# Kernel tuning notes

Measured on AMD Instinct MI355X. Metric: run time of the kernel, lower is better.

## Reference

```python
import jax, jax.numpy as jnp
import numpy as np
import math

H = 16
D_MODEL = 1024
D_K = D_MODEL // H


def setup_inputs() -> dict:
    key0 = jax.random.key(0)
    ks = jax.random.split(key0, 20)
    B, S, D = 4, 1024, D_MODEL
    inp = {
        'query': jax.random.normal(ks[0], (B, S, D), jnp.float32),
        'key': jax.random.normal(ks[1], (B, S, D), jnp.float32),
        'value': jax.random.normal(ks[2], (B, S, D), jnp.float32),
        'mask': jnp.ones((B, 1, S), jnp.int32),
    }
    sc = 1.0 / math.sqrt(D)
    # linears[0]=key proj, [1]=value proj, [2]=query proj, [3]=output proj (per source)
    names = ['W_k', 'W_v', 'W_q', 'W_o', 'W_fq', 'W_fg']
    for i, n in enumerate(names):
        inp[n] = jax.random.normal(ks[3 + i], (D, D), jnp.float32) * sc
        inp['b' + n[1:]] = jnp.zeros((D,), jnp.float32)
    inp['up'] = jax.random.normal(ks[10], (H, 1, D_K), jnp.float32) * sc
    inp['uz'] = jax.random.normal(ks[11], (H, 1, D_K), jnp.float32) * sc
    return inp


def _heads(x, B, S):
    return jnp.transpose(x.reshape(B, S, H, D_K), (0, 2, 1, 3))  # [B,h,S,d_k]


def reference(query, key, value, mask, W_k, b_k, W_v, b_v, W_q, b_q, W_o, b_o, W_fq, b_fq, W_fg, b_fg, up, uz):
    B, S, D = query.shape
    k = _heads(key @ W_k.T + b_k, B, S)
    v = _heads(value @ W_v.T + b_v, B, S)
    q_lin = query @ W_q.T + b_q  # [B,S,D]
    # Gaussian focus bias
    glo = jnp.mean(q_lin, axis=1, keepdims=True)  # [B,1,D]
    c = jnp.tanh(q_lin @ W_fq.T + b_fq + (glo @ W_fg.T + b_fg))
    c = _heads(c, B, S)  # [B,h,S,d_k]
    p = jnp.sum(c * up, axis=-1)  # [B,h,S]
    z = jnp.sum(c * uz, axis=-1)
    P = jax.nn.sigmoid(p) * S
    Z = jax.nn.sigmoid(z) * S
    j = jnp.arange(S, dtype=P.dtype)  # key positions
    G = -((j[None, None, None, :] - P[..., None]) ** 2) * 2.0 / (Z[..., None] ** 2)  # [B,h,S,S]
    q = _heads(q_lin, B, S)
    scores = jnp.einsum('bhqd,bhkd->bhqk', q, k) / math.sqrt(D_K) + G
    scores = jnp.where(mask[:, None] == 0, jnp.float32(-1e15), scores)
    attn = jax.nn.softmax(scores, axis=-1)
    x = jnp.einsum('bhqk,bhkd->bhqd', attn, v)
    x = jnp.transpose(x, (0, 2, 1, 3)).reshape(B, S, D)
    out = x @ W_o.T + b_o
    return out, jnp.mean(attn, axis=1)
```

## Files before the change

kernel.cpp:

```cpp
#include <hip/hip_runtime.h>
#include <hip/hip_bf16.h>
#include <math.h>

typedef __attribute__((ext_vector_type(8))) short short8;
typedef __attribute__((ext_vector_type(4))) short short4v;
typedef __attribute__((ext_vector_type(4))) float f32x4;
typedef unsigned short u16;

#define SC2 0.18033688011112042f
#define L2E 1.4426950408889634f

__device__ __forceinline__ u16 f2bf(float f) {
  union { float f; unsigned u; } v; v.f = f;
  unsigned u = v.u + 0x7fffu + ((v.u >> 16) & 1u);
  return (u16)(u >> 16);
}
__device__ __forceinline__ float bf2f(u16 h) {
  union { unsigned u; float f; } v; v.u = ((unsigned)h) << 16;
  return v.f;
}
__device__ __forceinline__ float fexp2(float x) {
  float r; asm("v_exp_f32 %0, %1" : "=v"(r) : "v"(x)); return r;
}
__device__ __forceinline__ void gl_lds16(const u16* g, u16* l) {
  __builtin_amdgcn_global_load_lds(
      (const __attribute__((address_space(1))) void*)g,
      (__attribute__((address_space(3))) void*)l, 16, 0, 0);
}

__device__ __forceinline__ size_t KFoff(int b, int h, int j, int d) {
  return ((((size_t)(b * 16 + h) * 64 + (j >> 4)) * 2 + (d >> 5)) * 64
          + ((d >> 3) & 3) * 16 + (j & 15)) * 8 + (d & 7);
}
__device__ __forceinline__ size_t VFoff(int b, int h, int j, int d) {
  return ((((size_t)(b * 16 + h) * 4 + (d >> 4)) * 32 + (j >> 5)) * 64
          + ((j >> 3) & 3) * 16 + (d & 15)) * 8 + (j & 7);
}

__global__ __launch_bounds__(256) void cvt_all(
    const float* __restrict__ q, const float* __restrict__ k, const float* __restrict__ v,
    const float* __restrict__ w0, const float* __restrict__ w1, const float* __restrict__ w2,
    const float* __restrict__ w3, const float* __restrict__ w4,
    u16* __restrict__ qb, u16* __restrict__ kb, u16* __restrict__ vb,
    u16* __restrict__ w0b, u16* __restrict__ w1b, u16* __restrict__ w2b,
    u16* __restrict__ w3b, u16* __restrict__ w4b) {
  int bid = blockIdx.x;
  const float* s; u16* d; int base;
  if (bid < 2048)      { s = q; d = qb; base = bid; }
  else if (bid < 4096) { s = k; d = kb; base = bid - 2048; }
  else if (bid < 6144) { s = v; d = vb; base = bid - 4096; }
  else {
    int t2 = bid - 6144; int wi = t2 >> 9; base = t2 & 511;
    if (wi == 0)      { s = w0; d = w0b; }
    else if (wi == 1) { s = w1; d = w1b; }
    else if (wi == 2) { s = w2; d = w2b; }
    else if (wi == 3) { s = w3; d = w3b; }
    else              { s = w4; d = w4b; }
  }
  size_t idx = (size_t)base * 2048 + (size_t)threadIdx.x * 8;
  float4 a = *(const float4*)(s + idx);
  float4 b = *(const float4*)(s + idx + 4);
  short8 o;
  o[0] = (short)f2bf(a.x); o[1] = (short)f2bf(a.y); o[2] = (short)f2bf(a.z); o[3] = (short)f2bf(a.w);
  o[4] = (short)f2bf(b.x); o[5] = (short)f2bf(b.y); o[6] = (short)f2bf(b.z); o[7] = (short)f2bf(b.w);
  *(short8*)(d + idx) = o;
}

#define GEMM_CORE(A_, Bw_)                                                              \
  f32x4 acc[4][4];                                                                      \
  _Pragma("unroll") for (int m = 0; m < 4; ++m)                                         \
    _Pragma("unroll") for (int n = 0; n < 4; ++n)                                       \
      acc[m][n] = (f32x4){0.f, 0.f, 0.f, 0.f};                                          \
  for (int k0 = 0; k0 < 1024; k0 += 64) {                                               \
    _Pragma("unroll") for (int p = 0; p < 4; ++p) {                                     \
      int idx = p * 256 + tid;                                                          \
      int row = idx >> 3, slot = idx & 7;                                               \
      gl_lds16(A_ + (size_t)(m0 + row) * 1024 + k0 + ((slot ^ (row & 7)) * 8), As + idx * 8); \
    }                                                                                   \
    _Pragma("unroll") for (int p = 0; p < 4; ++p) {                                     \
      int idx = p * 256 + tid;                                                          \
      int row = idx >> 3, slot = idx & 7;                                               \
      gl_lds16(Bw_ + (size_t)(n0 + row) * 1024 + k0 + ((slot ^ (row & 7)) * 8), Bs + idx * 8); \
    }                                                                                   \
    __syncthreads();                                                                    \
    _Pragma("unroll") for (int kk = 0; kk < 2; ++kk) {                                  \
      short8 af[4], bf[4];                                                              \
      _Pragma("unroll") for (int m = 0; m < 4; ++m) {                                   \
        int row = wrow + m * 16 + c;                                                    \
        af[m] = *(const short8*)(As + row * 64 + (((kk * 4 + g) ^ (row & 7)) * 8));     \
      }                                                                                 \
      _Pragma("unroll") for (int n = 0; n < 4; ++n) {                                   \
        int row = wcol + n * 16 + c;                                                    \
        bf[n] = *(const short8*)(Bs + row * 64 + (((kk * 4 + g) ^ (row & 7)) * 8));     \
      }                                                                                 \
      _Pragma("unroll") for (int m = 0; m < 4; ++m)                                     \
        _Pragma("unroll") for (int n = 0; n < 4; ++n)                                   \
          acc[m][n] = __builtin_amdgcn_mfma_f32_16x16x32_bf16(af[m], bf[n], acc[m][n], 0, 0, 0); \
    }                                                                                   \
    __syncthreads();                                                                    \
  }

__global__ __launch_bounds__(256, 2)
void proj_qkv(const u16* __restrict__ qb, const u16* __restrict__ kb, const u16* __restrict__ vb,
              const u16* __restrict__ wqb, const u16* __restrict__ wkb, const u16* __restrict__ wvb,
              const float* __restrict__ bq, const float* __restrict__ bk, const float* __restrict__ bv,
              u16* __restrict__ Ql, u16* __restrict__ Kf, u16* __restrict__ Vf) {
  __shared__ u16 As[128 * 64];
  __shared__ u16 Bs[128 * 64];
  const int z = blockIdx.z;
  const u16* A  = (z == 0) ? kb : (z == 1) ? vb : qb;
  const u16* Bw = (z == 0) ? wkb : (z == 1) ? wvb : wqb;
  const float* bias = (z == 0) ? bk : (z == 1) ? bv : bq;
  const int tid = threadIdx.x;
  const int l = tid & 63, w = tid >> 6;
  const int m0 = blockIdx.x * 128, n0 = blockIdx.y * 128;
  const int wrow = (w & 1) * 64, wcol = (w >> 1) * 64;
  const int g = l >> 4, c = l & 15;

  GEMM_CORE(A, Bw)

#pragma unroll
  for (int n = 0; n < 4; ++n) {
    int col = n0 + wcol + n * 16 + c;
    float bv_ = bias[col];
    int hh = col >> 6, dd = col & 63;
#pragma unroll
    for (int m = 0; m < 4; ++m) {
#pragma unroll
      for (int r = 0; r < 4; ++r) {
        int rowg = m0 + wrow + m * 16 + g * 4 + r;
        float val = acc[m][n][r] + bv_;
        int bb = rowg >> 10, jj = rowg & 1023;
        if (z == 0)      Kf[KFoff(bb, hh, jj, dd)] = f2bf(val);
        else if (z == 1) Vf[VFoff(bb, hh, jj, dd)] = f2bf(val);
        else             Ql[(size_t)rowg * 1024 + col] = f2bf(val);
      }
    }
  }
}

__global__ __launch_bounds__(256, 2)
void gemm_tanh(const u16* __restrict__ A, const u16* __restrict__ Bw,
               const float* __restrict__ gb, u16* __restrict__ Cout) {
  __shared__ u16 As[128 * 64];
  __shared__ u16 Bs[128 * 64];
  const int tid = threadIdx.x;
  const int l = tid & 63, w = tid >> 6;
  const int m0 = blockIdx.x * 128, n0 = blockIdx.y * 128;
  const int wrow = (w & 1) * 64, wcol = (w >> 1) * 64;
  const int g = l >> 4, c = l & 15;

  GEMM_CORE(A, Bw)

#pragma unroll
  for (int n = 0; n < 4; ++n) {
    int col = n0 + wcol + n * 16 + c;
    float bv = gb[(m0 >> 10) * 1024 + col];
#pragma unroll
    for (int m = 0; m < 4; ++m) {
#pragma unroll
      for (int r = 0; r < 4; ++r) {
        int rowg = m0 + wrow + m * 16 + g * 4 + r;
        Cout[(size_t)rowg * 1024 + col] = f2bf(tanhf(acc[m][n][r] + bv));
      }
    }
  }
}

__global__ __launch_bounds__(128) void glo_part_k(const u16* __restrict__ qlin, float* __restrict__ gpart) {
  int b = blockIdx.x & 3, seg = blockIdx.x >> 2;
  int t = threadIdx.x;
  float acc[8] = {0, 0, 0, 0, 0, 0, 0, 0};
  for (int s = seg * 16; s < seg * 16 + 16; ++s) {
    short8 v = *(const short8*)(qlin + (size_t)(b * 1024 + s) * 1024 + t * 8);
#pragma unroll
    for (int j = 0; j < 8; ++j) acc[j] += bf2f((u16)v[j]);
  }
#pragma unroll
  for (int j = 0; j < 8; ++j) gpart[(size_t)(seg * 4 + b) * 1024 + t * 8 + j] = acc[j];
}

__global__ __launch_bounds__(128) void glo_reduce(const float* __restrict__ gpart, float* __restrict__ glo) {
  int b = blockIdx.x & 3, cc = blockIdx.x >> 2;
  int col = cc * 128 + threadIdx.x;
  float a[8] = {0, 0, 0, 0, 0, 0, 0, 0};
#pragma unroll
  for (int s8 = 0; s8 < 8; ++s8) {
#pragma unroll
    for (int s = 0; s < 8; ++s)
      a[s] += gpart[(size_t)((s8 * 8 + s) * 4 + b) * 1024 + col];
  }
  float t = ((a[0] + a[1]) + (a[2] + a[3])) + ((a[4] + a[5]) + (a[6] + a[7]));
  glo[b * 1024 + col] = t * (1.0f / 1024.0f);
}

__global__ __launch_bounds__(256) void gbias_k(const float* __restrict__ glo, const float* __restrict__ Wfg,
                                               const float* __restrict__ bfq, const float* __restrict__ bfg,
                                               float* __restrict__ gbias) {
  __shared__ float glo_l[4096];
  int tid = threadIdx.x;
  for (int idx = tid; idx < 4096; idx += 256) glo_l[idx] = glo[idx];
  __syncthreads();
  int w = tid >> 6, l = tid & 63;
#pragma unroll
  for (int i = 0; i < 4; ++i) {
    int n = blockIdx.x * 16 + w * 4 + i;
    float a0 = 0, a1 = 0, a2 = 0, a3 = 0;
#pragma unroll
    for (int kk = 0; kk < 4; ++kk) {
      int k = kk * 256 + l * 4;
      float4 wv = *(const float4*)(Wfg + (size_t)n * 1024 + k);
      float4 g0 = *(const float4*)(&glo_l[k]);
      float4 g1 = *(const float4*)(&glo_l[1024 + k]);
      float4 g2 = *(const float4*)(&glo_l[2048 + k]);
      float4 g3 = *(const float4*)(&glo_l[3072 + k]);
      a0 += wv.x * g0.x + wv.y * g0.y + wv.z * g0.z + wv.w * g0.w;
      a1 += wv.x * g1.x + wv.y * g1.y + wv.z * g1.z + wv.w * g1.w;
      a2 += wv.x * g2.x + wv.y * g2.y + wv.z * g2.z + wv.w * g2.w;
      a3 += wv.x * g3.x + wv.y * g3.y + wv.z * g3.z + wv.w * g3.w;
    }
#pragma unroll
    for (int d = 1; d < 64; d <<= 1) {
      a0 += __shfl_xor(a0, d); a1 += __shfl_xor(a1, d);
      a2 += __shfl_xor(a2, d); a3 += __shfl_xor(a3, d);
    }
    if (l == 0) {
      float bb = bfq[n] + bfg[n];
      gbias[n] = a0 + bb; gbias[1024 + n] = a1 + bb;
      gbias[2048 + n] = a2 + bb; gbias[3072 + n] = a3 + bb;
    }
  }
}

__global__ __launch_bounds__(256) void pz_kernel(const u16* __restrict__ cbuf,
                                                 const float* __restrict__ up, const float* __restrict__ uz,
                                                 float* __restrict__ Pout, float* __restrict__ IZout) {
  __shared__ float lup[1024], luz[1024];
  int tid = threadIdx.x;
  for (int i = tid; i < 1024; i += 256) { lup[i] = up[i]; luz[i] = uz[i]; }
  __syncthreads();
  int w = tid >> 6, l = tid & 63;
  int sg = blockIdx.x * 4 + w;
  int b = sg >> 10, s = sg & 1023;
  const u16* crow = cbuf + (size_t)sg * 1024;
  for (int h = 0; h < 16; ++h) {
    float cv = bf2f(crow[h * 64 + l]);
    float pp = cv * lup[h * 64 + l];
    float zz = cv * luz[h * 64 + l];
#pragma unroll
    for (int d = 1; d < 64; d <<= 1) { pp += __shfl_xor(pp, d); zz += __shfl_xor(zz, d); }
    if (l == 0) {
      float Pv = 1024.f / (1.f + __expf(-pp));
      float Zv = 1024.f / (1.f + __expf(-zz));
      size_t o = (size_t)(b * 16 + h) * 1024 + s;
      Pout[o] = Pv;
      IZout[o] = 2.0f / (Zv * Zv) * L2E;
    }
  }
}

template<int WP>
__global__ __launch_bounds__(512, 4)
void attn_flash(const u16* __restrict__ Qlin, const u16* __restrict__ Kf, const u16* __restrict__ Vf,
                const float* __restrict__ Pbuf, const float* __restrict__ IZbuf,
                const int* __restrict__ mask,
                u16* __restrict__ xbuf, float* __restrict__ Mbuf, float* __restrict__ iLbuf,
                u16* __restrict__ Pall, float* __restrict__ mch) {
  __shared__ u16 sm16[24576];
  __shared__ float maskb_s[1024];

  const int tid = threadIdx.x;
  const int l = tid & 63, w = tid >> 6;
  const int g = l >> 4, c = l & 15;
  const int bid = blockIdx.x;
  const int bh = (bid & 7) + ((bid >> 6) << 3);
  const int qc = (bid >> 3) & 7;
  const int b = bh >> 4, h = bh & 15;
  const int q0w = qc * 128 + w * 16;

  char* ps_ = (char*)(sm16 + 16384) + w * 2048;

  const u16* KfH = Kf + (size_t)bh * 65536;
  const u16* VfH = Vf + (size_t)bh * 65536;
  const int sdt = tid >> 7, sinner = tid & 127;

#pragma unroll
  for (int i = 0; i < 2; ++i) {
    int idx = i * 512 + tid;
    maskb_s[idx] = (mask[b * 1024 + idx] == 0) ? -1.4e15f : 0.0f;
  }

  const u16* qrow = Qlin + (size_t)(b * 1024 + q0w + c) * 1024 + h * 64 + g * 8;
  short8 af0 = *(const short8*)qrow;
  short8 af1 = *(const short8*)(qrow + 32);
  float Pq[4], IZq[4];
#pragma unroll
  for (int r = 0; r < 4; ++r) {
    size_t o = (size_t)bh * 1024 + q0w + g * 4 + r;
    Pq[r] = Pbuf[o]; IZq[r] = IZbuf[o];
  }

  float m[4], lsum[4];
  f32x4 xacc[4];
#pragma unroll
  for (int r = 0; r < 4; ++r) { m[r] = -3.0e38f; lsum[r] = 0.f; }
#pragma unroll
  for (int dt = 0; dt < 4; ++dt) xacc[dt] = (f32x4){0.f, 0.f, 0.f, 0.f};

  gl_lds16(KfH + (size_t)0 * 4096 + tid * 8, sm16 + tid * 8);
  gl_lds16(VfH + ((size_t)(sdt * 32 + 0) * 512) + sinner * 8, sm16 + 4096 + tid * 8);
  __syncthreads();

  for (int jc = 0; jc < 16; ++jc) {
    const int bi = jc & 1;
    u16* Ksb = sm16 + bi * 8192;
    u16* Vsb = Ksb + 4096;
    if (jc < 15) {
      u16* Ksn = sm16 + (bi ^ 1) * 8192;
      gl_lds16(KfH + (size_t)(jc + 1) * 4096 + tid * 8, Ksn + tid * 8);
      gl_lds16(VfH + ((size_t)(sdt * 32 + (jc + 1) * 2) * 512) + sinner * 8, Ksn + 4096 + tid * 8);
    }

    f32x4 sc[4];
    float cm[4] = {-3.0e38f, -3.0e38f, -3.0e38f, -3.0e38f};
#pragma unroll
    for (int t = 0; t < 4; ++t) {
      short8 b0 = *(const short8*)(Ksb + (t * 2 + 0) * 512 + l * 8);
      short8 b1 = *(const short8*)(Ksb + (t * 2 + 1) * 512 + l * 8);
      f32x4 z = (f32x4){0.f, 0.f, 0.f, 0.f};
      z = __builtin_amdgcn_mfma_f32_16x16x32_bf16(af0, b0, z, 0, 0, 0);
      z = __builtin_amdgcn_mfma_f32_16x16x32_bf16(af1, b1, z, 0, 0, 0);
      int j = jc * 64 + t * 16 + c;
      float jf = (float)j, mbv = maskb_s[j];
#pragma unroll
      for (int r = 0; r < 4; ++r) {
        float diff = jf - Pq[r];
        float s = z[r] * SC2 + mbv - diff * diff * IZq[r];
        sc[t][r] = s;
        cm[r] = fmaxf(cm[r], s);
      }
    }
#pragma unroll
    for (int d = 1; d < 16; d <<= 1)
#pragma unroll
      for (int r = 0; r < 4; ++r) cm[r] = fmaxf(cm[r], __shfl_xor(cm[r], d));
    bool grow = (cm[0] > m[0]) | (cm[1] > m[1]) | (cm[2] > m[2]) | (cm[3] > m[3]);
    const bool resc = __any(grow);
    float scale[4], ps[4];
    if (resc) {
#pragma unroll
      for (int r = 0; r < 4; ++r) {
        float nm = fmaxf(m[r], cm[r]);
        scale[r] = fexp2(m[r] - nm);
        m[r] = nm;
      }
    }
#pragma unroll
    for (int r = 0; r < 4; ++r) ps[r] = 0.f;
#pragma unroll
    for (int t = 0; t < 4; ++t) {
#pragma unroll
      for (int r = 0; r < 4; ++r) {
        float p = fexp2(sc[t][r] - m[r]);
        ps[r] += p;
        int row = g * 4 + r;
        int byte = (row * 128 + (t * 16 + c) * 2) ^ ((row & 7) << 4);
        *(u16*)(ps_ + byte) = f2bf(p);
      }
    }
    if (resc) {
#pragma unroll
      for (int r = 0; r < 4; ++r) {
        lsum[r] = lsum[r] * scale[r] + ps[r];
#pragma unroll
        for (int dt = 0; dt < 4; ++dt) xacc[dt][r] *= scale[r];
      }
    } else {
#pragma unroll
      for (int r = 0; r < 4; ++r) lsum[r] += ps[r];
    }
    if (WP && c == 0) {
#pragma unroll
      for (int r = 0; r < 4; ++r)
        mch[((size_t)bh * 16 + jc) * 1024 + q0w + g * 4 + r] = m[r];
    }
    if (WP) {
#pragma unroll
      for (int k2 = 0; k2 < 2; ++k2) {
        int i = k2 * 512 + l * 8;
        int row = i >> 6, col = i & 63;
        int byte = (row * 128 + col * 2) ^ ((row & 7) << 4);
        short8 v = *(const short8*)(ps_ + byte);
        *(short8*)(Pall + (((size_t)bh * 16 + jc) * 1024 + q0w + row) * 64 + col) = v;
      }
    }
    short8 pa[2];
#pragma unroll
    for (int ks = 0; ks < 2; ++ks) {
      int abyte = (c * 128 + (ks * 32 + g * 8) * 2) ^ ((c & 7) << 4);
      pa[ks] = *(const short8*)(ps_ + abyte);
    }
#pragma unroll
    for (int dt = 0; dt < 4; ++dt) {
#pragma unroll
      for (int ks = 0; ks < 2; ++ks) {
        short8 vb = *(const short8*)(Vsb + (dt * 2 + ks) * 512 + l * 8);
        xacc[dt] = __builtin_amdgcn_mfma_f32_16x16x32_bf16(pa[ks], vb, xacc[dt], 0, 0, 0);
      }
    }
    __syncthreads();
  }

#pragma unroll
  for (int d = 1; d < 16; d <<= 1)
#pragma unroll
    for (int r = 0; r < 4; ++r) lsum[r] += __shfl_xor(lsum[r], d);
  float iLr[4];
#pragma unroll
  for (int r = 0; r < 4; ++r) iLr[r] = 1.0f / lsum[r];
  if (c == 0) {
#pragma unroll
    for (int r = 0; r < 4; ++r) {
      size_t o = (size_t)bh * 1024 + q0w + g * 4 + r;
      Mbuf[o] = m[r];
      iLbuf[o] = iLr[r];
    }
  }
  float* xs = (float*)sm16 + w * 1024;
#pragma unroll
  for (int dt = 0; dt < 4; ++dt)
#pragma unroll
    for (int r = 0; r < 4; ++r)
      xs[(g * 4 + r) * 64 + dt * 16 + c] = xacc[dt][r] * iLr[r];
#pragma unroll
  for (int k2 = 0; k2 < 4; ++k2) {
    int i = k2 * 256 + l * 4;
    int row = i >> 6, d0 = i & 63;
    f32x4 xv = *(const f32x4*)(xs + i);
    short4v o;
    o[0] = (short)f2bf(xv.x); o[1] = (short)f2bf(xv.y);
    o[2] = (short)f2bf(xv.z); o[3] = (short)f2bf(xv.w);
    *(short4v*)(xbuf + (size_t)(b * 1024 + q0w + row) * 1024 + h * 64 + d0) = o;
  }
}

__global__ __launch_bounds__(256, 2)
void epilogue_k(const u16* __restrict__ A, const u16* __restrict__ Bw,
                const float* __restrict__ bias, float* __restrict__ out0,
                const u16* __restrict__ Pall, const float* __restrict__ iLbuf,
                const float* __restrict__ Mbuf, const float* __restrict__ mchb,
                float* __restrict__ out2, int usePall) {
  __shared__ u16 As[128 * 64];
  __shared__ u16 Bs[128 * 64];
  const int bid = blockIdx.x;
  const int tid = threadIdx.x;
  if (bid >= 256) {
    if (!usePall) return;
    int bq = (bid - 256) * 2 + (tid >> 7);
    int b = bq >> 10, q = bq & 1023;
    int j = (tid & 127) * 8;
    int jc = j >> 6, jin = j & 63;
    float acc[8] = {0, 0, 0, 0, 0, 0, 0, 0};
    for (int h = 0; h < 16; ++h) {
      int bh = b * 16 + h;
      float M = Mbuf[(size_t)bh * 1024 + q];
      float iLh = iLbuf[(size_t)bh * 1024 + q];
      float mc = mchb[((size_t)bh * 16 + jc) * 1024 + q];
      float f = fexp2(mc - M) * iLh;
      short8 p = *(const short8*)(Pall + (((size_t)bh * 16 + jc) * 1024 + q) * 64 + jin);
#pragma unroll
      for (int i = 0; i < 8; ++i) acc[i] = fmaf(bf2f((u16)p[i]), f, acc[i]);
    }
    float* dst = out2 + (size_t)bq * 1024 + j;
#pragma unroll
    for (int i = 0; i < 8; ++i) dst[i] = acc[i] * 0.0625f;
    return;
  }
  const int l = tid & 63, w = tid >> 6;
  const int m0 = (bid & 31) * 128, n0 = (bid >> 5) * 128;
  const int wrow = (w & 1) * 64, wcol = (w >> 1) * 64;
  const int g = l >> 4, c = l & 15;

  GEMM_CORE(A, Bw)

#pragma unroll
  for (int n = 0; n < 4; ++n) {
    int col = n0 + wcol + n * 16 + c;
    float bv = bias[col];
#pragma unroll
    for (int m = 0; m < 4; ++m) {
#pragma unroll
      for (int r = 0; r < 4; ++r) {
        int rowg = m0 + wrow + m * 16 + g * 4 + r;
        out0[(size_t)rowg * 1024 + col] = acc[m][n][r] + bv;
      }
    }
  }
}

__global__ __launch_bounds__(512, 4)
void attn_mean(const u16* __restrict__ Qlin, const u16* __restrict__ Kf,
               const float* __restrict__ Pbuf, const float* __restrict__ IZbuf,
               const float* __restrict__ Mbuf, const float* __restrict__ iLbuf,
               const int* __restrict__ mask,
               float* __restrict__ out2) {
  const int tid = threadIdx.x;
  const int l = tid & 63, w = tid >> 6;
  const int g = l >> 4, c = l & 15;
  int chunk = (blockIdx.x % 8) * 64 + blockIdx.x / 8;
  const int b = chunk >> 7;
  const int qt = (chunk & 127) >> 1;
  const int jh = chunk & 1;
  const int q0 = qt * 16;
  const int jbase = jh * 512 + w * 64;

  float mb[4];
#pragma unroll
  for (int t = 0; t < 4; ++t)
    mb[t] = (mask[b * 1024 + jbase + t * 16 + c] == 0) ? -1.4e15f : 0.0f;

  f32x4 macc[4];
#pragma unroll
  for (int t = 0; t < 4; ++t) macc[t] = (f32x4){0.f, 0.f, 0.f, 0.f};

  for (int h = 0; h < 16; ++h) {
    const u16* qrow = Qlin + (size_t)(b * 1024 + q0 + c) * 1024 + h * 64 + g * 8;
    short8 af0 = *(const short8*)qrow;
    short8 af1 = *(const short8*)(qrow + 32);
    const u16* kb2 = Kf + ((size_t)((b * 16 + h) * 64 + jh * 32 + w * 4) * 2) * 512 + l * 8;
    float Pq[4], IZq[4], Mq[4], iLq[4];
#pragma unroll
    for (int r = 0; r < 4; ++r) {
      size_t o = (size_t)(b * 16 + h) * 1024 + q0 + g * 4 + r;
      Pq[r] = Pbuf[o]; IZq[r] = IZbuf[o]; Mq[r] = Mbuf[o]; iLq[r] = iLbuf[o] * 0.0625f;
    }
#pragma unroll
    for (int t = 0; t < 4; ++t) {
      short8 bf0 = *(const short8*)(kb2 + t * 1024);
      short8 bf1 = *(const short8*)(kb2 + t * 1024 + 512);
      f32x4 z = (f32x4){0.f, 0.f, 0.f, 0.f};
      z = __builtin_amdgcn_mfma_f32_16x16x32_bf16(af0, bf0, z, 0, 0, 0);
      z = __builtin_amdgcn_mfma_f32_16x16x32_bf16(af1, bf1, z, 0, 0, 0);
      float jf = (float)(jbase + t * 16 + c);
#pragma unroll
      for (int r = 0; r < 4; ++r) {
        float diff = jf - Pq[r];
        float s = z[r] * SC2 + mb[t] - diff * diff * IZq[r];
        macc[t][r] += fexp2(s - Mq[r]) * iLq[r];
      }
    }
  }
#pragma unroll
  for (int t = 0; t < 4; ++t) {
#pragma unroll
    for (int r = 0; r < 4; ++r)
      out2[(size_t)(b * 1024 + q0 + g * 4 + r) * 1024 + jbase + t * 16 + c] = macc[t][r];
  }
}

extern "C" void kernel_launch(void* const* d_in, const int* in_sizes, int n_in,
                              void* d_out, int out_size, void* d_ws, size_t ws_size,
                              hipStream_t stream) {
  const float* q   = (const float*)d_in[0];
  const float* k   = (const float*)d_in[1];
  const float* v   = (const float*)d_in[2];
  const int*   msk = (const int*)d_in[3];
  const float* Wk  = (const float*)d_in[4];  const float* bk  = (const float*)d_in[5];
  const float* Wv  = (const float*)d_in[6];  const float* bv  = (const float*)d_in[7];
  const float* Wq  = (const float*)d_in[8];  const float* bq  = (const float*)d_in[9];
  const float* Wo  = (const float*)d_in[10]; const float* bo  = (const float*)d_in[11];
  const float* Wfq = (const float*)d_in[12]; const float* bfq = (const float*)d_in[13];
  const float* Wfg = (const float*)d_in[14]; const float* bfg = (const float*)d_in[15];
  const float* up  = (const float*)d_in[16]; const float* uz  = (const float*)d_in[17];

  const size_t MB = 1u << 20;
  char* base = (char*)d_ws;
  char* p = base;
  auto take = [&](size_t n) { char* r = p; p += (n + 255) & ~(size_t)255; return r; };
  u16* Kf   = (u16*)take(8 * MB);
  u16* Ql   = (u16*)take(8 * MB);
  u16* Vf   = (u16*)take(8 * MB);
  u16* xb   = (u16*)take(8 * MB);
  u16* wob  = (u16*)take(2 * MB);
  float* Pb    = (float*)take((size_t)65536 * 4);
  float* IZb   = (float*)take((size_t)65536 * 4);
  float* Mb    = (float*)take((size_t)65536 * 4);
  float* iLb   = (float*)take((size_t)65536 * 4);
  float* mch   = (float*)take((size_t)64 * 16 * 1024 * 4);
  float* gpart = (float*)take((size_t)64 * 4 * 1024 * 4);
  float* glo   = (float*)take(4096 * 4);
  float* gbias = (float*)take(4096 * 4);
  size_t pool_off = (size_t)(p - base);
  u16* qb   = (u16*)take(8 * MB);
  u16* kb   = (u16*)take(8 * MB);
  u16* vb   = (u16*)take(8 * MB);
  u16* wkb  = (u16*)take(2 * MB);
  u16* wvb  = (u16*)take(2 * MB);
  u16* wqb  = (u16*)take(2 * MB);
  u16* wfqb = (u16*)take(2 * MB);
  u16* Cc   = (u16*)take(8 * MB);
  u16* Pall = (u16*)(base + pool_off);
  int usePall = (ws_size >= pool_off + (size_t)128 * MB) ? 1 : 0;

  float* out0 = (float*)d_out;
  float* out2 = out0 + (size_t)4 * 1024 * 1024;

  cvt_all<<<8704, 256, 0, stream>>>(q, k, v, Wk, Wv, Wq, Wfq, Wo,
                                    qb, kb, vb, wkb, wvb, wqb, wfqb, wob);
  dim3 gg3(32, 8, 3);
  proj_qkv<<<gg3, 256, 0, stream>>>(qb, kb, vb, wqb, wkb, wvb, bq, bk, bv, Ql, Kf, Vf);
  dim3 gg(32, 8);
  glo_part_k<<<256, 128, 0, stream>>>(Ql, gpart);
  glo_reduce<<<32, 128, 0, stream>>>(gpart, glo);
  gbias_k<<<64, 256, 0, stream>>>(glo, Wfg, bfq, bfg, gbias);
  gemm_tanh<<<gg, 256, 0, stream>>>(Ql, wfqb, gbias, Cc);
  pz_kernel<<<1024, 256, 0, stream>>>(Cc, up, uz, Pb, IZb);
  if (usePall) {
    attn_flash<1><<<512, 512, 0, stream>>>(Ql, Kf, Vf, Pb, IZb, msk, xb, Mb, iLb, Pall, mch);
    epilogue_k<<<2304, 256, 0, stream>>>(xb, wob, bo, out0, Pall, iLb, Mb, mch, out2, 1);
  } else {
    attn_flash<0><<<512, 512, 0, stream>>>(Ql, Kf, Vf, Pb, IZb, msk, xb, Mb, iLb, Pall, mch);
    attn_mean<<<512, 512, 0, stream>>>(Ql, Kf, Pb, IZb, Mb, iLb, msk, out2);
    epilogue_k<<<256, 256, 0, stream>>>(xb, wob, bo, out0, Pall, iLb, Mb, mch, out2, 0);
  }
}
```

Baseline: 202.2 us.

## Fold Gaussian bias and mask into an extra MFMA via augmented K/Q

Attention scores get the Gaussian focus bias and the mask added through the matrix unit instead of per-element VALU math. K gains a third 32-wide slice holding (j-512)^2, (j-512), 1 and the mask bias, filled by a new kaug_fill kernel. Each query row gets a matching coefficient vector (-IZ, 2·P·IZ, -P^2·IZ, 1), and the 1/sqrt(d_k)·log2e scale is folded into K at projection time. The flash loop also always rescales instead of branching on a max increase, and raises wave priority around the MFMA sections. The cost is 1.5x larger K tiles and more LDS. Rounding the large quadratic coefficients to bf16 may hurt accuracy of the bias term.

Result: no change. 200.2 us (-1.0%).

```diff
diff --git a/kernel.cpp b/kernel.cpp
--- a/kernel.cpp
+++ b/kernel.cpp
@@ -29,7 +29,7 @@
 }
 
 __device__ __forceinline__ size_t KFoff(int b, int h, int j, int d) {
-  return ((((size_t)(b * 16 + h) * 64 + (j >> 4)) * 2 + (d >> 5)) * 64
+  return ((((size_t)(b * 16 + h) * 64 + (j >> 4)) * 3 + (d >> 5)) * 64
           + ((d >> 3) & 3) * 16 + (j & 15)) * 8 + (d & 7);
 }
 __device__ __forceinline__ size_t VFoff(int b, int h, int j, int d) {
@@ -64,6 +64,27 @@
   o[0] = (short)f2bf(a.x); o[1] = (short)f2bf(a.y); o[2] = (short)f2bf(a.z); o[3] = (short)f2bf(a.w);
   o[4] = (short)f2bf(b.x); o[5] = (short)f2bf(b.y); o[6] = (short)f2bf(b.z); o[7] = (short)f2bf(b.w);
   *(short8*)(d + idx) = o;
+}
+
+__global__ __launch_bounds__(256) void kaug_fill(const int* __restrict__ mask, u16* __restrict__ Kf) {
+  int bidx = blockIdx.x;
+  int b = bidx >> 6, jt = bidx & 63;
+  int t = threadIdx.x;
+  int h = t >> 4, jj = t & 15;
+  int j = jt * 16 + jj;
+  float jc = (float)(j - 512);
+  float mbv = (mask[b * 1024 + j] == 0) ? -1.4e15f : 0.0f;
+  u16* base = Kf + ((size_t)((b * 16 + h) * 64 + jt) * 3 + 2) * 512;
+  short8 z8 = (short8){0, 0, 0, 0, 0, 0, 0, 0};
+  short8 f8 = z8;
+  f8[0] = (short)f2bf(jc * jc);
+  f8[1] = (short)f2bf(jc);
+  f8[2] = (short)f2bf(1.0f);
+  f8[3] = (short)f2bf(mbv);
+  *(short8*)(base + jj * 8) = f8;
+  *(short8*)(base + 128 + jj * 8) = z8;
+  *(short8*)(base + 256 + jj * 8) = z8;
+  *(short8*)(base + 384 + jj * 8) = z8;
 }
 
 #define GEMM_CORE(A_, Bw_)                                                              \
@@ -131,7 +152,7 @@
         int rowg = m0 + wrow + m * 16 + g * 4 + r;
         float val = acc[m][n][r] + bv_;
         int bb = rowg >> 10, jj = rowg & 1023;
-        if (z == 0)      Kf[KFoff(bb, hh, jj, dd)] = f2bf(val);
+        if (z == 0)      Kf[KFoff(bb, hh, jj, dd)] = f2bf(val * SC2);
         else if (z == 1) Vf[VFoff(bb, hh, jj, dd)] = f2bf(val);
         else             Ql[(size_t)rowg * 1024 + col] = f2bf(val);
       }
@@ -263,11 +284,9 @@
 __global__ __launch_bounds__(512, 4)
 void attn_flash(const u16* __restrict__ Qlin, const u16* __restrict__ Kf, const u16* __restrict__ Vf,
                 const float* __restrict__ Pbuf, const float* __restrict__ IZbuf,
-                const int* __restrict__ mask,
                 u16* __restrict__ xbuf, float* __restrict__ Mbuf, float* __restrict__ iLbuf,
                 u16* __restrict__ Pall, float* __restrict__ mch) {
-  __shared__ u16 sm16[24576];
-  __shared__ float maskb_s[1024];
+  __shared__ u16 sm16[28672];
 
   const int tid = threadIdx.x;
   const int l = tid & 63, w = tid >> 6;
@@ -278,26 +297,22 @@
   const int b = bh >> 4, h = bh & 15;
   const int q0w = qc * 128 + w * 16;
 
-  char* ps_ = (char*)(sm16 + 16384) + w * 2048;
-
-  const u16* KfH = Kf + (size_t)bh * 65536;
+  char* ps_ = (char*)(sm16 + 20480) + w * 2048;
+
+  const u16* KfH = Kf + (size_t)bh * 98304;
   const u16* VfH = Vf + (size_t)bh * 65536;
-  const int sdt = tid >> 7, sinner = tid & 127;
-
-#pragma unroll
-  for (int i = 0; i < 2; ++i) {
-    int idx = i * 512 + tid;
-    maskb_s[idx] = (mask[b * 1024 + idx] == 0) ? -1.4e15f : 0.0f;
-  }
 
   const u16* qrow = Qlin + (size_t)(b * 1024 + q0w + c) * 1024 + h * 64 + g * 8;
   short8 af0 = *(const short8*)qrow;
   short8 af1 = *(const short8*)(qrow + 32);
-  float Pq[4], IZq[4];
-#pragma unroll
-  for (int r = 0; r < 4; ++r) {
-    size_t o = (size_t)bh * 1024 + q0w + g * 4 + r;
-    Pq[r] = Pbuf[o]; IZq[r] = IZbuf[o];
+  short8 af2 = (short8){0, 0, 0, 0, 0, 0, 0, 0};
+  if (g == 0) {
+    float Pc = Pbuf[(size_t)bh * 1024 + q0w + c] - 512.0f;
+    float Ic = IZbuf[(size_t)bh * 1024 + q0w + c];
+    af2[0] = (short)f2bf(-Ic);
+    af2[1] = (short)f2bf(2.0f * Pc * Ic);
+    af2[2] = (short)f2bf(-Pc * Pc * Ic);
+    af2[3] = (short)f2bf(1.0f);
   }
 
   float m[4], lsum[4];
@@ -307,56 +322,56 @@
 #pragma unroll
   for (int dt = 0; dt < 4; ++dt) xacc[dt] = (f32x4){0.f, 0.f, 0.f, 0.f};
 
-  gl_lds16(KfH + (size_t)0 * 4096 + tid * 8, sm16 + tid * 8);
-  gl_lds16(VfH + ((size_t)(sdt * 32 + 0) * 512) + sinner * 8, sm16 + 4096 + tid * 8);
+  auto stage = [&](int jn, u16* nb) {
+    gl_lds16(KfH + (size_t)jn * 6144 + tid * 8, nb + tid * 8);
+    if (tid < 256) {
+      gl_lds16(KfH + (size_t)jn * 6144 + (512 + tid) * 8, nb + (512 + tid) * 8);
+      int v = tid + 256;
+      gl_lds16(VfH + ((size_t)((v >> 7) * 32 + jn * 2) * 512) + (v & 127) * 8, nb + 6144 + v * 8);
+    } else {
+      int v = tid - 256;
+      gl_lds16(VfH + ((size_t)((v >> 7) * 32 + jn * 2) * 512) + (v & 127) * 8, nb + 6144 + v * 8);
+    }
+  };
+
+  stage(0, sm16);
   __syncthreads();
 
   for (int jc = 0; jc < 16; ++jc) {
     const int bi = jc & 1;
-    u16* Ksb = sm16 + bi * 8192;
-    u16* Vsb = Ksb + 4096;
-    if (jc < 15) {
-      u16* Ksn = sm16 + (bi ^ 1) * 8192;
-      gl_lds16(KfH + (size_t)(jc + 1) * 4096 + tid * 8, Ksn + tid * 8);
-      gl_lds16(VfH + ((size_t)(sdt * 32 + (jc + 1) * 2) * 512) + sinner * 8, Ksn + 4096 + tid * 8);
-    }
+    u16* Ksb = sm16 + bi * 10240;
+    u16* Vsb = Ksb + 6144;
+    if (jc < 15) stage(jc + 1, sm16 + (bi ^ 1) * 10240);
 
     f32x4 sc[4];
     float cm[4] = {-3.0e38f, -3.0e38f, -3.0e38f, -3.0e38f};
+    __builtin_amdgcn_s_setprio(1);
 #pragma unroll
     for (int t = 0; t < 4; ++t) {
-      short8 b0 = *(const short8*)(Ksb + (t * 2 + 0) * 512 + l * 8);
-      short8 b1 = *(const short8*)(Ksb + (t * 2 + 1) * 512 + l * 8);
+      short8 b0 = *(const short8*)(Ksb + (t * 3 + 0) * 512 + l * 8);
+      short8 b1 = *(const short8*)(Ksb + (t * 3 + 1) * 512 + l * 8);
+      short8 b2 = *(const short8*)(Ksb + (t * 3 + 2) * 512 + l * 8);
       f32x4 z = (f32x4){0.f, 0.f, 0.f, 0.f};
       z = __builtin_amdgcn_mfma_f32_16x16x32_bf16(af0, b0, z, 0, 0, 0);
       z = __builtin_amdgcn_mfma_f32_16x16x32_bf16(af1, b1, z, 0, 0, 0);
-      int j = jc * 64 + t * 16 + c;
-      float jf = (float)j, mbv = maskb_s[j];
-#pragma unroll
-      for (int r = 0; r < 4; ++r) {
-        float diff = jf - Pq[r];
-        float s = z[r] * SC2 + mbv - diff * diff * IZq[r];
-        sc[t][r] = s;
-        cm[r] = fmaxf(cm[r], s);
-      }
-    }
+      z = __builtin_amdgcn_mfma_f32_16x16x32_bf16(af2, b2, z, 0, 0, 0);
+      sc[t] = z;
+#pragma unroll
+      for (int r = 0; r < 4; ++r) cm[r] = fmaxf(cm[r], z[r]);
+    }
+    __builtin_amdgcn_s_setprio(0);
 #pragma unroll
     for (int d = 1; d < 16; d <<= 1)
 #pragma unroll
       for (int r = 0; r < 4; ++r) cm[r] = fmaxf(cm[r], __shfl_xor(cm[r], d));
-    bool grow = (cm[0] > m[0]) | (cm[1] > m[1]) | (cm[2] > m[2]) | (cm[3] > m[3]);
-    const bool resc = __any(grow);
     float scale[4], ps[4];
-    if (resc) {
-#pragma unroll
-      for (int r = 0; r < 4; ++r) {
-        float nm = fmaxf(m[r], cm[r]);
-        scale[r] = fexp2(m[r] - nm);
-        m[r] = nm;
-      }
-    }
-#pragma unroll
-    for (int r = 0; r < 4; ++r) ps[r] = 0.f;
+#pragma unroll
+    for (int r = 0; r < 4; ++r) {
+      float nm = fmaxf(m[r], cm[r]);
+      scale[r] = fexp2(m[r] - nm);
+      m[r] = nm;
+      ps[r] = 0.f;
+    }
 #pragma unroll
     for (int t = 0; t < 4; ++t) {
 #pragma unroll
@@ -368,16 +383,11 @@
         *(u16*)(ps_ + byte) = f2bf(p);
       }
     }
-    if (resc) {
-#pragma unroll
-      for (int r = 0; r < 4; ++r) {
-        lsum[r] = lsum[r] * scale[r] + ps[r];
-#pragma unroll
-        for (int dt = 0; dt < 4; ++dt) xacc[dt][r] *= scale[r];
-      }
-    } else {
-#pragma unroll
-      for (int r = 0; r < 4; ++r) lsum[r] += ps[r];
+#pragma unroll
+    for (int r = 0; r < 4; ++r) {
+      lsum[r] = lsum[r] * scale[r] + ps[r];
+#pragma unroll
+      for (int dt = 0; dt < 4; ++dt) xacc[dt][r] *= scale[r];
     }
     if (WP && c == 0) {
 #pragma unroll
@@ -400,6 +410,7 @@
       int abyte = (c * 128 + (ks * 32 + g * 8) * 2) ^ ((c & 7) << 4);
       pa[ks] = *(const short8*)(ps_ + abyte);
     }
+    __builtin_amdgcn_s_setprio(1);
 #pragma unroll
     for (int dt = 0; dt < 4; ++dt) {
 #pragma unroll
@@ -408,6 +419,7 @@
         xacc[dt] = __builtin_amdgcn_mfma_f32_16x16x32_bf16(pa[ks], vb, xacc[dt], 0, 0, 0);
       }
     }
+    __builtin_amdgcn_s_setprio(0);
     __syncthreads();
   }
 
@@ -527,7 +539,7 @@
     const u16* qrow = Qlin + (size_t)(b * 1024 + q0 + c) * 1024 + h * 64 + g * 8;
     short8 af0 = *(const short8*)qrow;
     short8 af1 = *(const short8*)(qrow + 32);
-    const u16* kb2 = Kf + ((size_t)((b * 16 + h) * 64 + jh * 32 + w * 4) * 2) * 512 + l * 8;
+    const u16* kb2 = Kf + ((size_t)((b * 16 + h) * 64 + jh * 32 + w * 4) * 3) * 512 + l * 8;
     float Pq[4], IZq[4], Mq[4], iLq[4];
 #pragma unroll
     for (int r = 0; r < 4; ++r) {
@@ -536,8 +548,8 @@
     }
 #pragma unroll
     for (int t = 0; t < 4; ++t) {
-      short8 bf0 = *(const short8*)(kb2 + t * 1024);
-      short8 bf1 = *(const short8*)(kb2 + t * 1024 + 512);
+      short8 bf0 = *(const short8*)(kb2 + (t * 3 + 0) * 512);
+      short8 bf1 = *(const short8*)(kb2 + (t * 3 + 1) * 512);
       f32x4 z = (f32x4){0.f, 0.f, 0.f, 0.f};
       z = __builtin_amdgcn_mfma_f32_16x16x32_bf16(af0, bf0, z, 0, 0, 0);
       z = __builtin_amdgcn_mfma_f32_16x16x32_bf16(af1, bf1, z, 0, 0, 0);
@@ -545,7 +557,7 @@
 #pragma unroll
       for (int r = 0; r < 4; ++r) {
         float diff = jf - Pq[r];
-        float s = z[r] * SC2 + mb[t] - diff * diff * IZq[r];
+        float s = z[r] + mb[t] - diff * diff * IZq[r];
         macc[t][r] += fexp2(s - Mq[r]) * iLq[r];
       }
     }
@@ -577,7 +589,7 @@
   char* base = (char*)d_ws;
   char* p = base;
   auto take = [&](size_t n) { char* r = p; p += (n + 255) & ~(size_t)255; return r; };
-  u16* Kf   = (u16*)take(8 * MB);
+  u16* Kf   = (u16*)take(12 * MB);
   u16* Ql   = (u16*)take(8 * MB);
   u16* Vf   = (u16*)take(8 * MB);
   u16* xb   = (u16*)take(8 * MB);
@@ -607,6 +619,7 @@
 
   cvt_all<<<8704, 256, 0, stream>>>(q, k, v, Wk, Wv, Wq, Wfq, Wo,
                                     qb, kb, vb, wkb, wvb, wqb, wfqb, wob);
+  kaug_fill<<<256, 256, 0, stream>>>(msk, Kf);
   dim3 gg3(32, 8, 3);
   proj_qkv<<<gg3, 256, 0, stream>>>(qb, kb, vb, wqb, wkb, wvb, bq, bk, bv, Ql, Kf, Vf);
   dim3 gg(32, 8);
@@ -616,10 +629,10 @@
   gemm_tanh<<<gg, 256, 0, stream>>>(Ql, wfqb, gbias, Cc);
   pz_kernel<<<1024, 256, 0, stream>>>(Cc, up, uz, Pb, IZb);
   if (usePall) {
-    attn_flash<1><<<512, 512, 0, stream>>>(Ql, Kf, Vf, Pb, IZb, msk, xb, Mb, iLb, Pall, mch);
+    attn_flash<1><<<512, 512, 0, stream>>>(Ql, Kf, Vf, Pb, IZb, xb, Mb, iLb, Pall, mch);
     epilogue_k<<<2304, 256, 0, stream>>>(xb, wob, bo, out0, Pall, iLb, Mb, mch, out2, 1);
   } else {
-    attn_flash<0><<<512, 512, 0, stream>>>(Ql, Kf, Vf, Pb, IZb, msk, xb, Mb, iLb, Pall, mch);
+    attn_flash<0><<<512, 512, 0, stream>>>(Ql, Kf, Vf, Pb, IZb, xb, Mb, iLb, Pall, mch);
     attn_mean<<<512, 512, 0, stream>>>(Ql, Kf, Pb, IZb, Mb, iLb, msk, out2);
     epilogue_k<<<256, 256, 0, stream>>>(xb, wob, bo, out0, Pall, iLb, Mb, mch, out2, 0);
   }
```
